# Kernel tuning notes

Hardware: AMD Instinct MI355X
Metric: run time of the kernel (lower is better)

## Reference

```python
import jax, jax.numpy as jnp
import numpy as np

B, NK, NQ, DK, DQ, H, DV = 16, 256, 256, 256, 256, 128, 256
MASK_VAL = -1000000.0

def setup_inputs() -> dict:
    key = jax.random.key(0)
    ks = jax.random.split(key, 7)
    return {
        "key": jax.random.normal(ks[0], (B, NK, DK), dtype=jnp.float32),
        "query": jax.random.normal(ks[1], (B, NQ, DQ), dtype=jnp.float32),
        "value": jax.random.normal(ks[2], (B, NQ, DV), dtype=jnp.float32),
        "valid_lens": jax.random.randint(ks[3], (B,), 1, NQ + 1, dtype=jnp.int32),
        "Wk": jax.random.normal(ks[4], (DK, H), dtype=jnp.float32) / np.sqrt(DK),
        "Wq": jax.random.normal(ks[5], (DQ, H), dtype=jnp.float32) / np.sqrt(DQ),
        "wv": jax.random.normal(ks[6], (H,), dtype=jnp.float32) / np.sqrt(H),
    }

def reference(key, query, value, valid_lens, Wk, Wq, wv):
    k = key @ Wk                      # (B, NK, H)
    q = query @ Wq                    # (B, NQ, H)
    # note: original unsqueezes key at dim 2, query at dim 1 -> (B, NK, NQ, H)
    feature = jnp.tanh(k[:, :, None, :] + q[:, None, :, :])
    scores = jnp.einsum('bkqh,h->bkq', feature, wv)   # (B, NK, NQ)
    # mask along last (query) axis per batch, as repeat_interleave does
    pos = jnp.arange(scores.shape[-1])[None, None, :]
    masked = jnp.where(pos < valid_lens[:, None, None], scores, MASK_VAL)
    attn = jax.nn.softmax(masked, axis=-1)            # (B, NK, NQ)
    return jnp.einsum('bkq,bqd->bkd', attn, value)    # (B, NK, DV)
```

## Files before the change

### kernel.cpp

```cpp
#include <hip/hip_runtime.h>

#define B_   16
#define NK_  256
#define NQ_  256
#define DK_  256
#define H_   128
#define DV_  256

#define C2X 2.8853900817779268f
#define L2E 1.4426950408889634f
#define MASKV -1.0e5f

typedef float f4 __attribute__((ext_vector_type(4)));

__device__ __forceinline__ float exp2_fast(float x) { return __builtin_amdgcn_exp2f(x); }
__device__ __forceinline__ float rcp_fast(float x)  { return __builtin_amdgcn_rcpf(x); }

__global__ __launch_bounds__(256) void proj_kernel(
    const float* __restrict__ key, const float* __restrict__ query,
    const float* __restrict__ Wk,  const float* __restrict__ Wq,
    float* __restrict__ kfE, float* __restrict__ qE4)
{
    __shared__ alignas(16) float A_s[32 * 256];
    __shared__ alignas(16) float W_s[64 * 128];

    const int blk = blockIdx.x;
    const int tid = threadIdx.x;
    const bool isQ = blk >= 128;
    const int rb = (blk & 127) * 32;

    const float* __restrict__ A = isQ ? query : key;
    const float* __restrict__ W = isQ ? Wq : Wk;

    {
        const f4* src = (const f4*)(A + (size_t)rb * DK_);
        f4* dst = (f4*)A_s;
#pragma unroll
        for (int j = 0; j < 8; ++j) dst[tid + 256 * j] = src[tid + 256 * j];
    }

    const int rg = (tid >> 5) * 4;
    const int c4 = (tid & 31) * 4;

    f4 acc[4];
#pragma unroll
    for (int r = 0; r < 4; ++r) acc[r] = (f4){0.f, 0.f, 0.f, 0.f};

    for (int kc = 0; kc < DK_; kc += 64) {
        __syncthreads();
        {
            const f4* wsrc = (const f4*)(W + (size_t)kc * H_);
            f4* wdst = (f4*)W_s;
#pragma unroll
            for (int j = 0; j < 8; ++j) wdst[tid + 256 * j] = wsrc[tid + 256 * j];
        }
        __syncthreads();
#pragma unroll 2
        for (int k = 0; k < 64; k += 4) {
            f4 w0 = *(const f4*)(W_s + (k + 0) * H_ + c4);
            f4 w1 = *(const f4*)(W_s + (k + 1) * H_ + c4);
            f4 w2 = *(const f4*)(W_s + (k + 2) * H_ + c4);
            f4 w3 = *(const f4*)(W_s + (k + 3) * H_ + c4);
#pragma unroll
            for (int r = 0; r < 4; ++r) {
                f4 a = *(const f4*)(A_s + (rg + r) * 256 + kc + k);
                acc[r] += a[0] * w0;
                acc[r] += a[1] * w1;
                acc[r] += a[2] * w2;
                acc[r] += a[3] * w3;
            }
        }
    }

    if (!isQ) {
        float* dst = kfE + (size_t)(rb + rg) * H_ + c4;
#pragma unroll
        for (int r = 0; r < 4; ++r) {
            f4 o;
#pragma unroll
            for (int cc = 0; cc < 4; ++cc) o[cc] = exp2_fast(C2X * acc[r][cc]);
            *(f4*)(dst + (size_t)r * H_) = o;
        }
    } else {
        const int b  = rb >> 8;
        const int q0 = (rb & 255) + rg;
        f4* dst = (f4*)qE4 + ((size_t)(b * 32 + (c4 >> 2))) * NQ_ + q0;
#pragma unroll
        for (int r = 0; r < 4; ++r) {
            f4 o;
#pragma unroll
            for (int cc = 0; cc < 4; ++cc) o[cc] = exp2_fast(C2X * acc[r][cc]);
            dst[r] = o;
        }
    }
}

__global__ __launch_bounds__(256) void attn_kernel(
    const float* __restrict__ kfE, const float* __restrict__ qE4,
    const float* __restrict__ value, const int* __restrict__ vlens,
    const float* __restrict__ wv, float* __restrict__ out)
{
    __shared__ alignas(16) float kf_s[4 * 132];
    __shared__ alignas(16) float wv2_s[128];
    __shared__ alignas(16) float at4_s[256 * 4];
    __shared__ alignas(16) float red_s[16 * 256];

    const int x   = blockIdx.x;
    const int qu  = x >> 8;
    const int xi  = x & 255;
    const int b   = (xi + (qu << 2)) & 15;
    const int kt  = (xi >> 4) + (qu << 4);
    const int k0  = kt << 2;
    const int tid = threadIdx.x;
    const int w   = tid >> 6;
    const int lane = tid & 63;
    const int valid  = vlens[b];
    const int nchunk = (valid + 63) >> 6;

    if (tid < 128) {
        const int k = tid >> 5, h4 = tid & 31;
        f4 v = ((const f4*)(kfE + ((size_t)(b * NK_ + k0 + k)) * H_))[h4];
        *(f4*)(kf_s + k * 132 + (h4 << 2)) = v;
    }
    if (tid < 32) {
        f4 wvv = ((const f4*)wv)[tid];
        ((f4*)wv2_s)[tid] = 2.f * wvv;
    }
    __syncthreads();

    float sumwv;
    {
        f4 sw = {0.f, 0.f, 0.f, 0.f};
#pragma unroll
        for (int i = 0; i < 32; ++i) sw += ((const f4*)wv)[i];
        sumwv = (sw[0] + sw[1]) + (sw[2] + sw[3]);
    }

    float accA[4], accB[4];
#pragma unroll
    for (int j = 0; j < 4; ++j) { accA[j] = 0.f; accB[j] = 0.f; }

    {
        const f4* eq0 = (const f4*)qE4 + (size_t)b * (32 * NQ_) + lane;
        const float* kb = kf_s + w * 132;

        auto run = [&](int NC) {
            const f4* eqp = eq0;
#pragma unroll 4
            for (int h4 = 0; h4 < 32; ++h4) {
                f4 ek = *(const f4*)(kb + (h4 << 2));
                f4 w2 = *(const f4*)(wv2_s + (h4 << 2));
#pragma unroll
                for (int j = 0; j < 4; ++j) {
                    if (j >= NC) break;
                    f4 eq = eqp[j << 6];
                    float t0 = fmaf(ek[0], eq[0], 1.f);
                    float t1 = fmaf(ek[1], eq[1], 1.f);
                    float t2 = fmaf(ek[2], eq[2], 1.f);
                    float t3 = fmaf(ek[3], eq[3], 1.f);
                    accA[j] = fmaf(w2[0], rcp_fast(t0), accA[j]);
                    accB[j] = fmaf(w2[1], rcp_fast(t1), accB[j]);
                    accA[j] = fmaf(w2[2], rcp_fast(t2), accA[j]);
                    accB[j] = fmaf(w2[3], rcp_fast(t3), accB[j]);
                }
                eqp += NQ_;
            }
        };
        switch (nchunk) {
            case 1: run(1); break;
            case 2: run(2); break;
            case 3: run(3); break;
            default: run(4); break;
        }
    }

    {
        float s[4];
#pragma unroll
        for (int j = 0; j < 4; ++j) {
            const int q = (j << 6) + lane;
            s[j] = (j < nchunk && q < valid) ? (sumwv - (accA[j] + accB[j])) : MASKV;
        }
        float m = fmaxf(fmaxf(s[0], s[1]), fmaxf(s[2], s[3]));
#pragma unroll
        for (int off = 32; off >= 1; off >>= 1)
            m = fmaxf(m, __shfl_xor(m, off, 64));
        float ssum = 0.f;
#pragma unroll
        for (int j = 0; j < 4; ++j) {
            s[j] = exp2_fast(L2E * (s[j] - m));
            ssum += s[j];
        }
#pragma unroll
        for (int off = 32; off >= 1; off >>= 1)
            ssum += __shfl_xor(ssum, off, 64);
        const float inv = rcp_fast(ssum);
#pragma unroll
        for (int j = 0; j < 4; ++j)
            at4_s[(((j << 6) + lane) << 2) + w] = s[j] * inv;
    }
    __syncthreads();

    {
        const int rq = tid >> 6;
        const int d4 = (tid & 63) << 2;
        const float* vb = value + (size_t)b * (NQ_ * DV_) + d4;
        f4 o0 = {0.f,0.f,0.f,0.f}, o1 = o0, o2 = o0, o3 = o0;
#pragma unroll 4
        for (int q = rq; q < valid; q += 4) {
            f4 v  = *(const f4*)(vb + (size_t)q * DV_);
            f4 a4 = *(const f4*)(at4_s + (q << 2));
            o0 += a4[0] * v;
            o1 += a4[1] * v;
            o2 += a4[2] * v;
            o3 += a4[3] * v;
        }
        float* rs = red_s + (rq << 10) + d4;
        *(f4*)(rs + 0)    = o0;
        *(f4*)(rs + 256)  = o1;
        *(f4*)(rs + 512)  = o2;
        *(f4*)(rs + 768)  = o3;
    }
    __syncthreads();

    {
        const int k  = tid >> 6;
        const int d4 = (tid & 63) << 2;
        const float* rs = red_s + (k << 8) + d4;
        f4 o = *(const f4*)(rs) + *(const f4*)(rs + 1024)
             + *(const f4*)(rs + 2048) + *(const f4*)(rs + 3072);
        *(f4*)(out + ((size_t)(b * NK_ + k0 + k)) * DV_ + d4) = o;
    }
}

extern "C" void kernel_launch(void* const* d_in, const int* in_sizes, int n_in,
                              void* d_out, int out_size, void* d_ws, size_t ws_size,
                              hipStream_t stream)
{
    const float* key   = (const float*)d_in[0];
    const float* query = (const float*)d_in[1];
    const float* value = (const float*)d_in[2];
    const int*   vlens = (const int*)  d_in[3];
    const float* Wk    = (const float*)d_in[4];
    const float* Wq    = (const float*)d_in[5];
    const float* wv    = (const float*)d_in[6];
    float* outp = (float*)d_out;

    float* kfE = (float*)d_ws;
    float* qE4 = kfE + (size_t)B_ * NK_ * H_;

    hipLaunchKernelGGL(proj_kernel, dim3(256), dim3(256), 0, stream,
                       key, query, Wk, Wq, kfE, qE4);
    hipLaunchKernelGGL(attn_kernel, dim3(1024), dim3(256), 0, stream,
                       kfE, qE4, value, vlens, wv, outp);
}
```

Before: 102.9 us.

## Process eight keys per block with register-cached query features and LDS atomics

The attention kernel now handles 8 key rows per block instead of 4, halving the grid to 512 blocks. Each wave takes one 64-query chunk, rotated across blocks, and loads its query exp-features into registers once to reuse them across all 8 keys. Previously every wave re-read all query chunks for its own key. Scores go to LDS, softmax runs per row, and the value product uses LDS atomicAdd for the cross-wave reduction. The aim is less global traffic for qE4 and value per output row, at the cost of higher register pressure, LDS atomics, and idle waves when valid lengths are short.

```diff
diff --git a/kernel.cpp b/kernel.cpp
--- a/kernel.cpp
+++ b/kernel.cpp
@@ -100,24 +100,25 @@
     const float* __restrict__ value, const int* __restrict__ vlens,
     const float* __restrict__ wv, float* __restrict__ out)
 {
-    __shared__ alignas(16) float kf_s[4 * 132];
+    __shared__ alignas(16) float sc_s[8 * 260];
+    __shared__ alignas(16) float kf_s[8 * 132];
     __shared__ alignas(16) float wv2_s[128];
-    __shared__ alignas(16) float at4_s[256 * 4];
-    __shared__ alignas(16) float red_s[16 * 256];
-
-    const int x   = blockIdx.x;
-    const int qu  = x >> 8;
-    const int xi  = x & 255;
-    const int b   = (xi + (qu << 2)) & 15;
-    const int kt  = (xi >> 4) + (qu << 4);
-    const int k0  = kt << 2;
-    const int tid = threadIdx.x;
-    const int w   = tid >> 6;
+    __shared__ alignas(16) float red_s[8 * 256];
+
+    const int x    = blockIdx.x;
+    const int qu   = x >> 7;
+    const int xi   = x & 127;
+    const int b    = (xi + (qu << 2)) & 15;
+    const int kt   = (xi >> 4) + (qu << 3);
+    const int k0   = kt << 3;
+    const int rot  = ((xi >> 4) + qu) & 3;
+    const int tid  = threadIdx.x;
+    const int w    = tid >> 6;
     const int lane = tid & 63;
     const int valid  = vlens[b];
     const int nchunk = (valid + 63) >> 6;
 
-    if (tid < 128) {
+    {
         const int k = tid >> 5, h4 = tid & 31;
         f4 v = ((const f4*)(kfE + ((size_t)(b * NK_ + k0 + k)) * H_))[h4];
         *(f4*)(kf_s + k * 132 + (h4 << 2)) = v;
@@ -126,7 +127,8 @@
         f4 wvv = ((const f4*)wv)[tid];
         ((f4*)wv2_s)[tid] = 2.f * wvv;
     }
-    __syncthreads();
+    ((f4*)red_s)[tid]       = (f4){0.f, 0.f, 0.f, 0.f};
+    ((f4*)red_s)[tid + 256] = (f4){0.f, 0.f, 0.f, 0.f};
 
     float sumwv;
     {
@@ -135,101 +137,112 @@
         for (int i = 0; i < 32; ++i) sw += ((const f4*)wv)[i];
         sumwv = (sw[0] + sw[1]) + (sw[2] + sw[3]);
     }
-
-    float accA[4], accB[4];
-#pragma unroll
-    for (int j = 0; j < 4; ++j) { accA[j] = 0.f; accB[j] = 0.f; }
-
-    {
-        const f4* eq0 = (const f4*)qE4 + (size_t)b * (32 * NQ_) + lane;
-        const float* kb = kf_s + w * 132;
-
-        auto run = [&](int NC) {
-            const f4* eqp = eq0;
-#pragma unroll 4
-            for (int h4 = 0; h4 < 32; ++h4) {
-                f4 ek = *(const f4*)(kb + (h4 << 2));
-                f4 w2 = *(const f4*)(wv2_s + (h4 << 2));
-#pragma unroll
-                for (int j = 0; j < 4; ++j) {
-                    if (j >= NC) break;
-                    f4 eq = eqp[j << 6];
-                    float t0 = fmaf(ek[0], eq[0], 1.f);
-                    float t1 = fmaf(ek[1], eq[1], 1.f);
-                    float t2 = fmaf(ek[2], eq[2], 1.f);
-                    float t3 = fmaf(ek[3], eq[3], 1.f);
-                    accA[j] = fmaf(w2[0], rcp_fast(t0), accA[j]);
-                    accB[j] = fmaf(w2[1], rcp_fast(t1), accB[j]);
-                    accA[j] = fmaf(w2[2], rcp_fast(t2), accA[j]);
-                    accB[j] = fmaf(w2[3], rcp_fast(t3), accB[j]);
+    __syncthreads();
+
+    {
+        const int c = (w + rot) & 3;
+        if (c < nchunk) {
+            const int q = (c << 6) + lane;
+            const f4* eqp = (const f4*)qE4 + (size_t)b * (32 * NQ_) + q;
+
+            float acc[8];
+#pragma unroll
+            for (int k = 0; k < 8; ++k) acc[k] = 0.f;
+
+#pragma unroll
+            for (int half = 0; half < 2; ++half) {
+                f4 eq[16];
+#pragma unroll
+                for (int i = 0; i < 16; ++i)
+                    eq[i] = eqp[(size_t)(half * 16 + i) * NQ_];
+#pragma unroll
+                for (int i = 0; i < 16; ++i) {
+                    const int h4 = (half * 16 + i) << 2;
+                    const f4 w4 = *(const f4*)(wv2_s + h4);
+                    const f4 e  = eq[i];
+#pragma unroll
+                    for (int k = 0; k < 8; ++k) {
+                        const f4 ek = *(const f4*)(kf_s + k * 132 + h4);
+                        acc[k] = fmaf(w4[0], rcp_fast(fmaf(ek[0], e[0], 1.f)), acc[k]);
+                        acc[k] = fmaf(w4[1], rcp_fast(fmaf(ek[1], e[1], 1.f)), acc[k]);
+                        acc[k] = fmaf(w4[2], rcp_fast(fmaf(ek[2], e[2], 1.f)), acc[k]);
+                        acc[k] = fmaf(w4[3], rcp_fast(fmaf(ek[3], e[3], 1.f)), acc[k]);
+                    }
                 }
-                eqp += NQ_;
-            }
-        };
-        switch (nchunk) {
-            case 1: run(1); break;
-            case 2: run(2); break;
-            case 3: run(3); break;
-            default: run(4); break;
-        }
-    }
-
-    {
-        float s[4];
-#pragma unroll
-        for (int j = 0; j < 4; ++j) {
-            const int q = (j << 6) + lane;
-            s[j] = (j < nchunk && q < valid) ? (sumwv - (accA[j] + accB[j])) : MASKV;
-        }
-        float m = fmaxf(fmaxf(s[0], s[1]), fmaxf(s[2], s[3]));
-#pragma unroll
-        for (int off = 32; off >= 1; off >>= 1)
-            m = fmaxf(m, __shfl_xor(m, off, 64));
-        float ssum = 0.f;
-#pragma unroll
-        for (int j = 0; j < 4; ++j) {
-            s[j] = exp2_fast(L2E * (s[j] - m));
-            ssum += s[j];
-        }
-#pragma unroll
-        for (int off = 32; off >= 1; off >>= 1)
-            ssum += __shfl_xor(ssum, off, 64);
-        const float inv = rcp_fast(ssum);
-#pragma unroll
-        for (int j = 0; j < 4; ++j)
-            at4_s[(((j << 6) + lane) << 2) + w] = s[j] * inv;
-    }
-    __syncthreads();
-
-    {
-        const int rq = tid >> 6;
-        const int d4 = (tid & 63) << 2;
+            }
+#pragma unroll
+            for (int k = 0; k < 8; ++k)
+                sc_s[k * 260 + q] = sumwv - acc[k];
+        }
+    }
+    __syncthreads();
+
+    {
+#pragma unroll
+        for (int kk = 0; kk < 2; ++kk) {
+            const int k = (w << 1) + kk;
+            float* row = sc_s + k * 260;
+            float s[4];
+            float m = MASKV;
+#pragma unroll
+            for (int j = 0; j < 4; ++j) {
+                const int q = (j << 6) + lane;
+                s[j] = (q < valid) ? row[q] : MASKV;
+                m = fmaxf(m, s[j]);
+            }
+#pragma unroll
+            for (int off = 32; off >= 1; off >>= 1)
+                m = fmaxf(m, __shfl_xor(m, off, 64));
+            float ssum = 0.f;
+#pragma unroll
+            for (int j = 0; j < 4; ++j) {
+                s[j] = exp2_fast(L2E * (s[j] - m));
+                ssum += s[j];
+            }
+#pragma unroll
+            for (int off = 32; off >= 1; off >>= 1)
+                ssum += __shfl_xor(ssum, off, 64);
+            const float inv = rcp_fast(ssum);
+#pragma unroll
+            for (int j = 0; j < 4; ++j)
+                row[(j << 6) + lane] = s[j] * inv;
+        }
+    }
+    __syncthreads();
+
+    {
+        const int d4 = lane << 2;
         const float* vb = value + (size_t)b * (NQ_ * DV_) + d4;
-        f4 o0 = {0.f,0.f,0.f,0.f}, o1 = o0, o2 = o0, o3 = o0;
-#pragma unroll 4
-        for (int q = rq; q < valid; q += 4) {
-            f4 v  = *(const f4*)(vb + (size_t)q * DV_);
-            f4 a4 = *(const f4*)(at4_s + (q << 2));
-            o0 += a4[0] * v;
-            o1 += a4[1] * v;
-            o2 += a4[2] * v;
-            o3 += a4[3] * v;
-        }
-        float* rs = red_s + (rq << 10) + d4;
-        *(f4*)(rs + 0)    = o0;
-        *(f4*)(rs + 256)  = o1;
-        *(f4*)(rs + 512)  = o2;
-        *(f4*)(rs + 768)  = o3;
-    }
-    __syncthreads();
-
-    {
-        const int k  = tid >> 6;
-        const int d4 = (tid & 63) << 2;
-        const float* rs = red_s + (k << 8) + d4;
-        f4 o = *(const f4*)(rs) + *(const f4*)(rs + 1024)
-             + *(const f4*)(rs + 2048) + *(const f4*)(rs + 3072);
-        *(f4*)(out + ((size_t)(b * NK_ + k0 + k)) * DV_ + d4) = o;
+        f4 o[8];
+#pragma unroll
+        for (int k = 0; k < 8; ++k) o[k] = (f4){0.f, 0.f, 0.f, 0.f};
+#pragma unroll 2
+        for (int q = w; q < valid; q += 4) {
+            const f4 v = *(const f4*)(vb + (size_t)q * DV_);
+#pragma unroll
+            for (int k = 0; k < 8; ++k)
+                o[k] += sc_s[k * 260 + q] * v;
+        }
+#pragma unroll
+        for (int k = 0; k < 8; ++k) {
+            float* p = red_s + (k << 8) + d4;
+            atomicAdd(p + 0, o[k][0]);
+            atomicAdd(p + 1, o[k][1]);
+            atomicAdd(p + 2, o[k][2]);
+            atomicAdd(p + 3, o[k][3]);
+        }
+    }
+    __syncthreads();
+
+    {
+#pragma unroll
+        for (int e = 0; e < 2; ++e) {
+            const int i  = tid + (e << 8);
+            const int k  = i >> 6;
+            const int dd = (i & 63) << 2;
+            f4 ov = *(const f4*)(red_s + (k << 8) + dd);
+            *(f4*)(out + ((size_t)(b * NK_ + k0 + k)) * DV_ + dd) = ov;
+        }
     }
 }
 
@@ -251,6 +264,6 @@
 
     hipLaunchKernelGGL(proj_kernel, dim3(256), dim3(256), 0, stream,
                        key, query, Wk, Wq, kfE, qE4);
-    hipLaunchKernelGGL(attn_kernel, dim3(1024), dim3(256), 0, stream,
+    hipLaunchKernelGGL(attn_kernel, dim3(512), dim3(256), 0, stream,
                        kfE, qE4, value, vlens, wv, outp);
 }
```

Measured after the change: 130.2 us. 26.5% more time.
